# Optimization experiments

Hardware: AMD Instinct MI355X
Metric: run time of the kernel (lower is better)

The kernel has to match this reference:

```python
import jax, jax.numpy as jnp
import numpy as np

B, M, L, HID, H, LAYERS = 16, 128, 512, 256, 4, 2
DH = HID // H  # 64 = head dim, also kernel_param dim


def _ln(x, g, b, eps=1e-5):
    mu = jnp.mean(x, axis=-1, keepdims=True)
    var = jnp.mean((x - mu) ** 2, axis=-1, keepdims=True)
    return (x - mu) / jnp.sqrt(var + eps) * g + b


def setup_inputs() -> dict:
    key = jax.random.key(0)
    ks = jax.random.split(key, 24)
    s = 0.05
    return {
        "ct_t": jax.random.uniform(ks[0], (B, M), jnp.float32),
        "ts_t": jax.random.uniform(ks[1], (B, L), jnp.float32),
        "ct_emb": jax.random.normal(ks[2], (B, M, HID), jnp.float32),
        "ts_emb": jax.random.normal(ks[3], (B, L, HID), jnp.float32),
        "kernel_param": jax.random.normal(ks[4], (DH,), jnp.float32),
        "ct_W": jax.random.normal(ks[5], (HID, HID), jnp.float32) * s,
        "ct_b": jnp.zeros((HID,), jnp.float32),
        "fW0": jax.random.normal(ks[6], (HID, HID), jnp.float32) * s,
        "fb0": jnp.zeros((HID,), jnp.float32),
        "fW1": jax.random.normal(ks[7], (HID, HID), jnp.float32) * s,
        "fb1": jnp.zeros((HID,), jnp.float32),
        "fW2": jax.random.normal(ks[8], (HID, HID), jnp.float32) * s,
        "fb2": jnp.zeros((HID,), jnp.float32),
        "f_ln_g": jnp.ones((HID,), jnp.float32),
        "f_ln_b": jnp.zeros((HID,), jnp.float32),
        "Wqkv": jax.random.normal(ks[9], (LAYERS, 3 * HID, HID), jnp.float32) * s,
        "bqkv": jnp.zeros((LAYERS, 3 * HID), jnp.float32),
        "Wo": jax.random.normal(ks[10], (LAYERS, HID, HID), jnp.float32) * s,
        "bo": jnp.zeros((LAYERS, HID), jnp.float32),
        "W1": jax.random.normal(ks[11], (LAYERS, 2 * HID, HID), jnp.float32) * s,
        "b1": jnp.zeros((LAYERS, 2 * HID), jnp.float32),
        "W2": jax.random.normal(ks[12], (LAYERS, HID, 2 * HID), jnp.float32) * s,
        "b2": jnp.zeros((LAYERS, HID), jnp.float32),
        "ln1_g": jnp.ones((LAYERS, HID), jnp.float32),
        "ln1_b": jnp.zeros((LAYERS, HID), jnp.float32),
        "ln2_g": jnp.ones((LAYERS, HID), jnp.float32),
        "ln2_b": jnp.zeros((LAYERS, HID), jnp.float32),
        "pred_W": jax.random.normal(ks[13], (1, HID), jnp.float32) * s,
        "pred_b": jnp.zeros((1,), jnp.float32),
    }


def reference(ct_t, ts_t, ct_emb, ts_emb, kernel_param, ct_W, ct_b,
              fW0, fb0, fW1, fb1, fW2, fb2, f_ln_g, f_ln_b,
              Wqkv, bqkv, Wo, bo, W1, b1, W2, b2,
              ln1_g, ln1_b, ln2_g, ln2_b, pred_W, pred_b):
    # --- TN tokenizer: multi-scale RBF kernel temporal fusion ---
    alpha = jax.nn.softplus(kernel_param)                       # [DH]  log(1+exp(p))
    ct_e = (jnp.einsum('bmd,ed->bme', ct_emb, ct_W) + ct_b)     # [B,M,HID]
    ct_e = ct_e.reshape(B, M, H, DH)
    diff = ct_t[:, :, None] - ts_t[:, None, :]                  # [B,M,L]
    norm = (diff * diff)[..., None]                             # [B,M,L,1]
    outs = []
    for s in range(H):                                          # fixed small loop over scales
        z = (-float(s)) * alpha * norm                          # [B,M,L,DH]
        w = jax.nn.logsumexp(z, axis=3, keepdims=True)          # [B,M,L,1]
        sim = jnp.exp(z - w)                                    # normalized kernel sims
        outs.append(jnp.einsum('bmnd,bmd->bnd', sim, ct_e[:, :, s, :]))  # scatter over ts events
    temp = jnp.concatenate(outs, axis=-1)                       # [B,L,HID]
    # --- Fusion module ---
    aux = jax.nn.elu(temp @ fW0.T + fb0 + ts_emb @ fW1.T + fb1)
    x = _ln(aux @ fW2.T + fb2 + ts_emb, f_ln_g, f_ln_b)         # [B,L,HID]
    # --- Transformer encoder (post-LN, gelu, no dropout at eval) ---
    inv_sqrt = 1.0 / np.sqrt(DH).astype(np.float32)
    for l in range(LAYERS):
        qkv = x @ Wqkv[l].T + bqkv[l]                           # [B,L,3*HID]
        q, k, v = jnp.split(qkv, 3, axis=-1)
        def heads(t):
            return t.reshape(B, L, H, DH).transpose(0, 2, 1, 3)
        q, k, v = heads(q), heads(k), heads(v)
        att = jax.nn.softmax(jnp.einsum('bhqd,bhkd->bhqk', q, k) * inv_sqrt, axis=-1)
        o = jnp.einsum('bhqk,bhkd->bhqd', att, v).transpose(0, 2, 1, 3).reshape(B, L, HID)
        x = _ln(x + o @ Wo[l].T + bo[l], ln1_g[l], ln1_b[l])
        ff = jax.nn.gelu(x @ W1[l].T + b1[l], approximate=False) @ W2[l].T + b2[l]
        x = _ln(x + ff, ln2_g[l], ln2_b[l])
    return x @ pred_W.T + pred_b                                # [B,L,1]
```

## Files before the change

### kernel.cpp

```cpp
#include <hip/hip_runtime.h>
#include <hip/hip_bf16.h>
#include <cstddef>

#define Bsz 16
#define Msz 128
#define Lsz 512
#define HIDs 256

typedef __attribute__((ext_vector_type(4))) float f32x4;
typedef __attribute__((ext_vector_type(8))) __bf16 bf16x8;
typedef __attribute__((ext_vector_type(8))) unsigned short ushort8;

#define CHEB_K 12
#define PI_F 3.14159265358979323846f

static __device__ inline unsigned short f2bf(float f) {
    __hip_bfloat16 h = __float2bfloat16(f);
    return *(unsigned short*)&h;
}
static __device__ inline float bf2f(unsigned short u) {
    return __builtin_bit_cast(float, (unsigned)u << 16);
}
static __device__ inline void gload16(const ushort* g, ushort* l) {
    __builtin_amdgcn_global_load_lds(
        (const __attribute__((address_space(1))) void*)g,
        (__attribute__((address_space(3))) void*)l, 16, 0, 0);
}

__global__ __launch_bounds__(256) void cvt_all_kernel(
    const float* __restrict__ ts_emb, const float* __restrict__ ct_emb,
    const float* __restrict__ ct_W, const float* __restrict__ fW0,
    const float* __restrict__ fW1, const float* __restrict__ fW2,
    const float* __restrict__ Wqkv, const float* __restrict__ Wo,
    const float* __restrict__ W1, const float* __restrict__ W2,
    ushort* __restrict__ Xcat, ushort* __restrict__ Wcat,
    ushort* __restrict__ cebin, ushort* __restrict__ wct,
    ushort* __restrict__ wf2, ushort* __restrict__ wqkv,
    ushort* __restrict__ wo, ushort* __restrict__ w1, ushort* __restrict__ w2)
{
    const unsigned u = blockIdx.x * 256u + threadIdx.x;
    const float* src; ushort* dst; unsigned rel;
    if (u < 262144u) {
        rel = u; src = ts_emb;
        dst = Xcat + ((size_t)(rel >> 5) * 512 + 256 + (rel & 31) * 8);
    } else if (u < 327680u) { rel = u - 262144u; src = ct_emb; dst = cebin + (size_t)rel * 8; }
    else if (u < 335872u) { rel = u - 327680u; src = ct_W; dst = wct + (size_t)rel * 8; }
    else if (u < 344064u) { rel = u - 335872u; src = fW0;
        dst = Wcat + ((size_t)(rel >> 5) * 512 + (rel & 31) * 8); }
    else if (u < 352256u) { rel = u - 344064u; src = fW1;
        dst = Wcat + ((size_t)(rel >> 5) * 512 + 256 + (rel & 31) * 8); }
    else if (u < 360448u) { rel = u - 352256u; src = fW2; dst = wf2 + (size_t)rel * 8; }
    else if (u < 409600u) { rel = u - 360448u; src = Wqkv; dst = wqkv + (size_t)rel * 8; }
    else if (u < 425984u) { rel = u - 409600u; src = Wo;  dst = wo + (size_t)rel * 8; }
    else if (u < 458752u) { rel = u - 425984u; src = W1;  dst = w1 + (size_t)rel * 8; }
    else                  { rel = u - 458752u; src = W2;  dst = w2 + (size_t)rel * 8; }
    float4 a = ((const float4*)src)[(size_t)rel * 2];
    float4 b = ((const float4*)src)[(size_t)rel * 2 + 1];
    ushort8 o;
    o[0] = f2bf(a.x); o[1] = f2bf(a.y); o[2] = f2bf(a.z); o[3] = f2bf(a.w);
    o[4] = f2bf(b.x); o[5] = f2bf(b.y); o[6] = f2bf(b.z); o[7] = f2bf(b.w);
    *(ushort8*)dst = o;
}

__global__ __launch_bounds__(256) void gemm_mfma_kernel(
    const ushort* __restrict__ X, const ushort* __restrict__ W,
    const float* __restrict__ bias, const float* __restrict__ bias2,
    float* __restrict__ Yf, ushort* __restrict__ Yb,
    int NR, int K, int OUT, int act)
{
    __shared__ ushort As[64 * 64];
    __shared__ ushort Bs[128 * 64];

    const int nbx = OUT >> 7;
    const int bx = blockIdx.x % nbx;
    const int by = blockIdx.x / nbx;
    const int r0 = by << 6, o0 = bx << 7;
    const int tid = threadIdx.x;
    const int w = tid >> 6;
    const int lane = tid & 63;
    const int wr = w >> 1, wc = w & 1;
    const int lr = lane & 15, lg = lane >> 4;

    const int grow = lane >> 3;
    const int gchunk = (lane & 7) ^ grow;

    unsigned aoff[2][2], boff[4][2];
    #pragma unroll
    for (int f = 0; f < 2; f++) {
        unsigned cc = (unsigned)((lg + 4 * f) ^ (lr & 7)) * 16u;
        #pragma unroll
        for (int m = 0; m < 2; m++)
            aoff[m][f] = (unsigned)(wr * 32 + m * 16 + lr) * 128u + cc;
        #pragma unroll
        for (int n = 0; n < 4; n++)
            boff[n][f] = (unsigned)(wc * 64 + n * 16 + lr) * 128u + cc;
    }

    f32x4 acc[2][4];
    #pragma unroll
    for (int m = 0; m < 2; m++)
        #pragma unroll
        for (int n = 0; n < 4; n++) acc[m][n] = (f32x4){0.f, 0.f, 0.f, 0.f};

    const int nk = K >> 6;
    for (int ks = 0; ks < nk; ks++) {
        const int k0 = ks << 6;
        if (ks) __syncthreads();
        #pragma unroll
        for (int i = 0; i < 2; i++) {
            int row = w * 16 + i * 8 + grow;
            gload16(X + (size_t)(r0 + row) * K + k0 + gchunk * 8,
                    &As[(w * 16 + i * 8) * 64]);
        }
        #pragma unroll
        for (int i = 0; i < 4; i++) {
            int row = w * 32 + i * 8 + grow;
            gload16(W + (size_t)(o0 + row) * K + k0 + gchunk * 8,
                    &Bs[(w * 32 + i * 8) * 64]);
        }
        __syncthreads();

        #pragma unroll
        for (int f = 0; f < 2; f++) {
            bf16x8 av[2], bv[4];
            #pragma unroll
            for (int m = 0; m < 2; m++)
                av[m] = *(const bf16x8*)((const char*)As + aoff[m][f]);
            #pragma unroll
            for (int n = 0; n < 4; n++)
                bv[n] = *(const bf16x8*)((const char*)Bs + boff[n][f]);
            #pragma unroll
            for (int m = 0; m < 2; m++)
                #pragma unroll
                for (int n = 0; n < 4; n++)
                    acc[m][n] = __builtin_amdgcn_mfma_f32_16x16x32_bf16(
                        av[m], bv[n], acc[m][n], 0, 0, 0);
        }
    }

    const int ocol0 = o0 + wc * 64;
    float bn[4];
    #pragma unroll
    for (int n = 0; n < 4; n++) {
        int o = ocol0 + n * 16 + lr;
        bn[n] = bias[o] + (bias2 ? bias2[o] : 0.f);
    }

    #pragma unroll
    for (int m = 0; m < 2; m++) {
        #pragma unroll
        for (int p = 0; p < 4; p++) {
            int r = r0 + wr * 32 + m * 16 + 4 * lg + p;
            size_t rb = (size_t)r * OUT;
            #pragma unroll
            for (int n = 0; n < 4; n++) {
                int o = ocol0 + n * 16 + lr;
                float v = acc[m][n][p] + bn[n];
                if (act == 1)      v = (v > 0.f) ? v : (__expf(v) - 1.f);
                else if (act == 2) v = 0.5f * v * (1.f + erff(v * 0.70710678118654752f));
                if (Yf) Yf[rb + o] = v;
                if (Yb) Yb[rb + o] = f2bf(v);
            }
        }
    }
}

__global__ __launch_bounds__(256) void gemm_ln_kernel(
    const ushort* __restrict__ X, const ushort* __restrict__ W,
    const float* __restrict__ bias, const float* __restrict__ add,
    const float* __restrict__ lng, const float* __restrict__ lnb,
    float* __restrict__ Xf, ushort* __restrict__ Xb,
    const float* __restrict__ predW, const float* __restrict__ predb,
    float* __restrict__ pout, int K)
{
    __shared__ ushort As[32 * 64];
    __shared__ ushort Bs[256 * 64];
    __shared__ float redA[32][4];
    __shared__ float redB[32][4];

    const int r0 = blockIdx.x << 5;
    const int tid = threadIdx.x;
    const int w = tid >> 6;
    const int lane = tid & 63;
    const int lr = lane & 15, lg = lane >> 4;
    const int grow = lane >> 3;
    const int gchunk = (lane & 7) ^ grow;

    unsigned aoff[2][2], boff[4][2];
    #pragma unroll
    for (int f = 0; f < 2; f++) {
        unsigned cc = (unsigned)((lg + 4 * f) ^ (lr & 7)) * 16u;
        #pragma unroll
        for (int m = 0; m < 2; m++)
            aoff[m][f] = (unsigned)(m * 16 + lr) * 128u + cc;
        #pragma unroll
        for (int n = 0; n < 4; n++)
            boff[n][f] = (unsigned)(w * 64 + n * 16 + lr) * 128u + cc;
    }

    f32x4 acc[2][4];
    #pragma unroll
    for (int m = 0; m < 2; m++)
        #pragma unroll
        for (int n = 0; n < 4; n++) acc[m][n] = (f32x4){0.f, 0.f, 0.f, 0.f};

    const int nk = K >> 6;
    for (int ks = 0; ks < nk; ks++) {
        const int k0 = ks << 6;
        if (ks) __syncthreads();
        gload16(X + (size_t)(r0 + w * 8 + grow) * K + k0 + gchunk * 8,
                &As[(w * 8) * 64]);
        #pragma unroll
        for (int i = 0; i < 8; i++) {
            gload16(W + (size_t)(w * 64 + i * 8 + grow) * K + k0 + gchunk * 8,
                    &Bs[(w * 64 + i * 8) * 64]);
        }
        __syncthreads();

        #pragma unroll
        for (int f = 0; f < 2; f++) {
            bf16x8 av[2], bv[4];
            #pragma unroll
            for (int m = 0; m < 2; m++)
                av[m] = *(const bf16x8*)((const char*)As + aoff[m][f]);
            #pragma unroll
            for (int n = 0; n < 4; n++)
                bv[n] = *(const bf16x8*)((const char*)Bs + boff[n][f]);
            #pragma unroll
            for (int m = 0; m < 2; m++)
                #pragma unroll
                for (int n = 0; n < 4; n++)
                    acc[m][n] = __builtin_amdgcn_mfma_f32_16x16x32_bf16(
                        av[m], bv[n], acc[m][n], 0, 0, 0);
        }
    }

    const int col0 = w * 64;
    float bn[4], gv[4], bv2[4], pwv[4];
    #pragma unroll
    for (int n = 0; n < 4; n++) {
        int o = col0 + n * 16 + lr;
        bn[n] = bias[o];
        gv[n] = lng[o];
        bv2[n] = lnb[o];
        pwv[n] = predW ? predW[o] : 0.f;
    }
    #pragma unroll
    for (int m = 0; m < 2; m++)
        #pragma unroll
        for (int p = 0; p < 4; p++) {
            int r = r0 + m * 16 + 4 * lg + p;
            size_t rb = (size_t)r * 256;
            #pragma unroll
            for (int n = 0; n < 4; n++)
                acc[m][n][p] += bn[n] + add[rb + col0 + n * 16 + lr];
        }

    #pragma unroll
    for (int m = 0; m < 2; m++)
        #pragma unroll
        for (int p = 0; p < 4; p++) {
            float s = acc[m][0][p] + acc[m][1][p] + acc[m][2][p] + acc[m][3][p];
            #pragma unroll
            for (int o = 1; o <= 8; o <<= 1) s += __shfl_xor(s, o);
            if (lr == 0) redA[m * 16 + 4 * lg + p][w] = s;
        }
    __syncthreads();
    float mu[2][4];
    #pragma unroll
    for (int m = 0; m < 2; m++)
        #pragma unroll
        for (int p = 0; p < 4; p++) {
            int row = m * 16 + 4 * lg + p;
            mu[m][p] = (redA[row][0] + redA[row][1] + redA[row][2] + redA[row][3])
                       * (1.f / 256.f);
        }

    #pragma unroll
    for (int m = 0; m < 2; m++)
        #pragma unroll
        for (int p = 0; p < 4; p++) {
            float q = 0.f;
            #pragma unroll
            for (int n = 0; n < 4; n++) {
                float dl = acc[m][n][p] - mu[m][p];
                q = fmaf(dl, dl, q);
            }
            #pragma unroll
            for (int o = 1; o <= 8; o <<= 1) q += __shfl_xor(q, o);
            if (lr == 0) redB[m * 16 + 4 * lg + p][w] = q;
        }
    __syncthreads();

    #pragma unroll
    for (int m = 0; m < 2; m++)
        #pragma unroll
        for (int p = 0; p < 4; p++) {
            int row = m * 16 + 4 * lg + p;
            float var = (redB[row][0] + redB[row][1] + redB[row][2] + redB[row][3])
                        * (1.f / 256.f);
            float rsig = rsqrtf(var + 1e-5f);
            int r = r0 + row;
            size_t rb = (size_t)r * 256;
            float pd = 0.f;
            #pragma unroll
            for (int n = 0; n < 4; n++) {
                int o = col0 + n * 16 + lr;
                float xn = (acc[m][n][p] - mu[m][p]) * rsig * gv[n] + bv2[n];
                if (Xf) Xf[rb + o] = xn;
                if (Xb) Xb[rb + o] = f2bf(xn);
                pd = fmaf(xn, pwv[n], pd);
            }
            if (predW) {
                #pragma unroll
                for (int o = 1; o <= 8; o <<= 1) pd += __shfl_xor(pd, o);
                if (lr == 0) redA[row][w] = pd;
            }
        }
    if (predW) {
        __syncthreads();
        if (tid < 32)
            pout[r0 + tid] = redA[tid][0] + redA[tid][1] + redA[tid][2]
                           + redA[tid][3] + predb[0];
    }
}

__global__ __launch_bounds__(256) void cheb_kernel(
    const float* __restrict__ kp, float* __restrict__ clut, float* __restrict__ cD)
{
    __shared__ float costab[CHEB_K][32];
    __shared__ float xq[32];
    __shared__ float alph[64];
    const int t = threadIdx.x;
    if (t < 64) {
        float p = kp[t];
        alph[t] = fmaxf(p, 0.f) + log1pf(__expf(-fabsf(p)));
    }
    #pragma unroll
    for (int i = 0; i < 2; i++) {
        int idx = i * 256 + t;
        if (idx < CHEB_K * 32) {
            int k = idx >> 5, q = idx & 31;
            float th = (q + 0.5f) * (PI_F / 32.f);
            costab[k][q] = __cosf((float)k * th);
        }
    }
    if (t < 32) xq[t] = 0.5f * (1.f + __cosf((t + 0.5f) * (PI_F / 32.f)));
    __syncthreads();

    if (t >= 192) return;
    const int d = t & 63, s1 = t >> 6;
    const float u = (float)(s1 + 1) * alph[d];
    float f[32];
    #pragma unroll
    for (int q = 0; q < 32; q++) f[q] = __expf(-u * xq[q]);
    #pragma unroll
    for (int k = 0; k < CHEB_K; k++) {
        float sum = 0.f;
        #pragma unroll
        for (int q = 0; q < 32; q++) sum = fmaf(f[q], costab[k][q], sum);
        float c = sum * ((k == 0 ? 1.f : 2.f) / 32.f);
        clut[s1 * (CHEB_K * 64) + k * 64 + d] = c;
        float sr = c;
        #pragma unroll
        for (int o = 1; o <= 32; o <<= 1) sr += __shfl_xor(sr, o, 64);
        if (d == 0) cD[s1 * CHEB_K + k] = sr;
    }
}

__global__ __launch_bounds__(256) void denom3_kernel(
    const float* __restrict__ ct_t, const float* __restrict__ ts_t,
    const float* __restrict__ cD, ushort* __restrict__ invW)
{
    __shared__ float cd[3][CHEB_K];
    const int tid = threadIdx.x;
    if (tid < 3 * CHEB_K) cd[tid / CHEB_K][tid % CHEB_K] = cD[tid];
    __syncthreads();

    const unsigned G = blockIdx.x * 256u + tid;
    const int b = G >> 16;
    const int n = (G >> 7) & 511;
    const int m = G & 127;

    float x = ct_t[b * Msz + m] - ts_t[b * Lsz + n];
    x = x * x;
    const float xi = 2.f * x - 1.f;
    const float xi2 = 2.f * xi;

    float t0 = 1.f, t1 = xi;
    float a1 = cd[0][0] + cd[0][1] * xi;
    float a2 = cd[1][0] + cd[1][1] * xi;
    float a3 = cd[2][0] + cd[2][1] * xi;
    #pragma unroll
    for (int k = 2; k < CHEB_K; k++) {
        float tn = fmaf(xi2, t1, -t0);
        a1 = fmaf(cd[0][k], tn, a1);
        a2 = fmaf(cd[1][k], tn, a2);
        a3 = fmaf(cd[2][k], tn, a3);
        t0 = t1; t1 = tn;
    }
    const size_t base = ((size_t)b * 3 * Lsz + n) * Msz + m;
    invW[base]                         = f2bf(1.f / a1);
    invW[base + (size_t)Lsz * Msz]     = f2bf(1.f / a2);
    invW[base + (size_t)2 * Lsz * Msz] = f2bf(1.f / a3);
}

__global__ __launch_bounds__(256) void tok3_kernel(
    const float* __restrict__ ct_t, const float* __restrict__ ts_t,
    const ushort* __restrict__ ceb, const ushort* __restrict__ invW,
    const float* __restrict__ clut, ushort* __restrict__ Xcat)
{
    const int bid = blockIdx.x;
    const int nt = bid & 7;
    const int s1 = (bid >> 3) % 3;
    const int b  = bid / 24;
    const int tid = threadIdx.x;
    const int w = tid >> 6, lane = tid & 63, g = lane >> 4, r = lane & 15;

    __shared__ ushort ceT[64][136];
    __shared__ float  cl[CHEB_K][64];
    __shared__ float  cts[128];

    #pragma unroll
    for (int i = 0; i < 8; i++) {
        int idx = i * 256 + tid;
        int m = idx >> 4, d4 = (idx & 15) << 2;
        const ushort* gp = ceb + (((size_t)b * 128 + m) << 8) + (s1 + 1) * 64 + d4;
        ushort4 v = *(const ushort4*)gp;
        ceT[d4 + 0][m] = v.x; ceT[d4 + 1][m] = v.y;
        ceT[d4 + 2][m] = v.z; ceT[d4 + 3][m] = v.w;
    }
    #pragma unroll
    for (int i = 0; i < 3; i++) {
        int idx = i * 256 + tid;
        cl[idx >> 6][idx & 63] = clut[s1 * (CHEB_K * 64) + idx];
    }
    if (tid < 128) cts[tid] = ct_t[b * 128 + tid];
    __syncthreads();

    const int nrow = nt * 64 + w * 16 + r;
    const float tsn = ts_t[b * 512 + nrow];

    float xi2v[4][8], Ta[4][8], Tb[4][8];
    #pragma unroll
    for (int t4 = 0; t4 < 4; t4++) {
        int m0 = 8 * g + 32 * t4;
        ushort8 iv = *(const ushort8*)&invW[((((size_t)b * 3 + s1) * 512 + nrow) << 7) + m0];
        #pragma unroll
        for (int j = 0; j < 8; j++) {
            float dfx = cts[m0 + j] - tsn;
            float x = dfx * dfx;
            float xi = 2.f * x - 1.f;
            float w0 = bf2f(iv[j]);
            xi2v[t4][j] = 2.f * xi;
            Ta[t4][j] = w0;
            Tb[t4][j] = w0 * xi;
        }
    }

    bf16x8 cef[4][4];
    #pragma unroll
    for (int db = 0; db < 4; db++)
        #pragma unroll
        for (int t4 = 0; t4 < 4; t4++)
            cef[db][t4] = *(const bf16x8*)&ceT[db * 16 + r][8 * g + 32 * t4];

    f32x4 acc[4];
    #pragma unroll
    for (int db = 0; db < 4; db++) acc[db] = (f32x4){0.f, 0.f, 0.f, 0.f};

    #pragma unroll
    for (int k = 0; k < CHEB_K; k++) {
        if (k >= 2) {
            #pragma unroll
            for (int t4 = 0; t4 < 4; t4++)
                #pragma unroll
                for (int j = 0; j < 8; j++) {
                    if (k & 1) Tb[t4][j] = fmaf(xi2v[t4][j], Ta[t4][j], -Tb[t4][j]);
                    else       Ta[t4][j] = fmaf(xi2v[t4][j], Tb[t4][j], -Ta[t4][j]);
                }
        }
        bf16x8 af[4];
        #pragma unroll
        for (int t4 = 0; t4 < 4; t4++) {
            ushort8 u;
            #pragma unroll
            for (int j = 0; j < 8; j++)
                u[j] = f2bf((k & 1) ? Tb[t4][j] : Ta[t4][j]);
            af[t4] = __builtin_bit_cast(bf16x8, u);
        }
        #pragma unroll
        for (int db = 0; db < 4; db++) {
            f32x4 gk = (f32x4){0.f, 0.f, 0.f, 0.f};
            #pragma unroll
            for (int t4 = 0; t4 < 4; t4++)
                gk = __builtin_amdgcn_mfma_f32_16x16x32_bf16(af[t4], cef[db][t4], gk, 0, 0, 0);
            float ck = cl[k][db * 16 + r];
            #pragma unroll
            for (int p = 0; p < 4; p++) acc[db][p] = fmaf(ck, gk[p], acc[db][p]);
        }
    }

    #pragma unroll
    for (int db = 0; db < 4; db++)
        #pragma unroll
        for (int p = 0; p < 4; p++) {
            int n_out = nt * 64 + w * 16 + 4 * g + p;
            Xcat[((size_t)b * 512 + n_out) * 512 + (s1 + 1) * 64 + db * 16 + r] =
                f2bf(acc[db][p]);
        }
}

__global__ __launch_bounds__(256) void bcast0_kernel(
    const ushort* __restrict__ ceb, ushort* __restrict__ Xcat)
{
    const int b = blockIdx.x;
    const int t = threadIdx.x;
    const int d = t & 63, q = t >> 6;
    float s = 0.f;
    #pragma unroll 8
    for (int i = 0; i < 32; i++) {
        int m = q * 32 + i;
        s += bf2f(ceb[(((size_t)b * 128 + m) << 8) + d]);
    }
    __shared__ float red[4][64];
    __shared__ ushort row[64];
    red[q][d] = s;
    __syncthreads();
    if (t < 64)
        row[t] = f2bf((red[0][t] + red[1][t] + red[2][t] + red[3][t]) * (1.f / 64.f));
    __syncthreads();
    #pragma unroll
    for (int i = 0; i < 16; i++) {
        int idx = i * 256 + t;
        int n = idx >> 3, j = idx & 7;
        *(ushort8*)&Xcat[((size_t)b * 512 + n) * 512 + j * 8] =
            *(const ushort8*)&row[j * 8];
    }
}

__global__ __launch_bounds__(256) void attn_mfma_kernel(
    const ushort* __restrict__ qkv, ushort* __restrict__ Ob)
{
    const int bid = blockIdx.x;
    const int qt = bid & 7;
    const int h  = (bid >> 3) & 3;
    const int b  = bid >> 5;
    const int t  = threadIdx.x;
    const int w  = t >> 6;
    const int lane = t & 63;
    const int g = lane >> 4;
    const int r = lane & 15;

    __shared__ ushort Ks[64][72];
    __shared__ ushort Vt[64][72];
    __shared__ float  Ps[4][16][65];

    const ushort* base = qkv + (size_t)b * Lsz * 768;
    const int q0 = qt * 64 + w * 16;

    bf16x8 qf[2];
    {
        const ushort* qp = base + (size_t)(q0 + r) * 768 + h * 64 + 8 * g;
        qf[0] = __builtin_bit_cast(bf16x8, *(const ushort8*)qp);
        qf[1] = __builtin_bit_cast(bf16x8, *(const ushort8*)(qp + 32));
    }

    f32x4 Ofr[4];
    #pragma unroll
    for (int dblk = 0; dblk < 4; dblk++) Ofr[dblk] = (f32x4){0.f, 0.f, 0.f, 0.f};
    float m_run[4] = {-1e30f, -1e30f, -1e30f, -1e30f};
    float l_run[4] = {0.f, 0.f, 0.f, 0.f};

    const int srow = t >> 2;
    const int sseg = t & 3;

    for (int c = 0; c < 8; c++) {
        __syncthreads();
        {
            const ushort* kr = base + (size_t)(c * 64 + srow) * 768 + 256 + h * 64 + sseg * 16;
            ushort8 k0 = *(const ushort8*)kr;
            ushort8 k1 = *(const ushort8*)(kr + 8);
            *(ushort8*)&Ks[srow][sseg * 16]     = k0;
            *(ushort8*)&Ks[srow][sseg * 16 + 8] = k1;
            ushort8 v0 = *(const ushort8*)(kr + 256);
            ushort8 v1 = *(const ushort8*)(kr + 264);
            #pragma unroll
            for (int j = 0; j < 8; j++) {
                Vt[sseg * 16 + j][srow]     = v0[j];
                Vt[sseg * 16 + 8 + j][srow] = v1[j];
            }
        }
        __syncthreads();

        f32x4 sfr[4];
        #pragma unroll
        for (int s = 0; s < 4; s++) {
            f32x4 a2 = (f32x4){0.f, 0.f, 0.f, 0.f};
            #pragma unroll
            for (int f = 0; f < 2; f++) {
                bf16x8 kf = *(const bf16x8*)&Ks[s * 16 + r][8 * g + 32 * f];
                a2 = __builtin_amdgcn_mfma_f32_16x16x32_bf16(qf[f], kf, a2, 0, 0, 0);
            }
            #pragma unroll
            for (int p = 0; p < 4; p++) a2[p] *= 0.125f;
            sfr[s] = a2;
        }

        #pragma unroll
        for (int p = 0; p < 4; p++) {
            float rm = fmaxf(fmaxf(sfr[0][p], sfr[1][p]), fmaxf(sfr[2][p], sfr[3][p]));
            #pragma unroll
            for (int o = 1; o <= 8; o <<= 1) rm = fmaxf(rm, __shfl_xor(rm, o));
            float mnew = fmaxf(m_run[p], rm);
            float sc = __expf(m_run[p] - mnew);
            m_run[p] = mnew;
            float rs = 0.f;
            #pragma unroll
            for (int s = 0; s < 4; s++) {
                float pv = __expf(sfr[s][p] - mnew);
                Ps[w][4 * g + p][s * 16 + r] = pv;
                rs += pv;
            }
            #pragma unroll
            for (int o = 1; o <= 8; o <<= 1) rs += __shfl_xor(rs, o);
            l_run[p] = l_run[p] * sc + rs;
            #pragma unroll
            for (int dblk = 0; dblk < 4; dblk++) Ofr[dblk][p] *= sc;
        }

        __asm__ volatile("s_waitcnt lgkmcnt(0)" ::: "memory");

        #pragma unroll
        for (int f = 0; f < 2; f++) {
            const float* pp = &Ps[w][r][8 * g + 32 * f];
            ushort8 ua;
            #pragma unroll
            for (int j = 0; j < 8; j++) ua[j] = f2bf(pp[j]);
            bf16x8 pa = __builtin_bit_cast(bf16x8, ua);
            #pragma unroll
            for (int dblk = 0; dblk < 4; dblk++) {
                bf16x8 vb = *(const bf16x8*)&Vt[dblk * 16 + r][32 * f + 8 * g];
                Ofr[dblk] = __builtin_amdgcn_mfma_f32_16x16x32_bf16(
                    pa, vb, Ofr[dblk], 0, 0, 0);
            }
        }
    }

    #pragma unroll
    for (int dblk = 0; dblk < 4; dblk++) {
        #pragma unroll
        for (int p = 0; p < 4; p++) {
            int row = q0 + 4 * g + p;
            Ob[(size_t)(b * Lsz + row) * HIDs + h * 64 + dblk * 16 + r] =
                f2bf(Ofr[dblk][p] / l_run[p]);
        }
    }
}

extern "C" void kernel_launch(void* const* d_in, const int* in_sizes, int n_in,
                              void* d_out, int out_size, void* d_ws, size_t ws_size,
                              hipStream_t stream)
{
    (void)in_sizes; (void)n_in; (void)out_size; (void)ws_size;

    const float* ct_t   = (const float*)d_in[0];
    const float* ts_t   = (const float*)d_in[1];
    const float* ct_emb = (const float*)d_in[2];
    const float* ts_emb = (const float*)d_in[3];
    const float* kp     = (const float*)d_in[4];
    const float* ct_W   = (const float*)d_in[5];
    const float* ct_b   = (const float*)d_in[6];
    const float* fW0    = (const float*)d_in[7];
    const float* fb0    = (const float*)d_in[8];
    const float* fW1    = (const float*)d_in[9];
    const float* fb1    = (const float*)d_in[10];
    const float* fW2    = (const float*)d_in[11];
    const float* fb2    = (const float*)d_in[12];
    const float* f_ln_g = (const float*)d_in[13];
    const float* f_ln_b = (const float*)d_in[14];
    const float* Wqkv   = (const float*)d_in[15];
    const float* bqkv   = (const float*)d_in[16];
    const float* Wo     = (const float*)d_in[17];
    const float* bo     = (const float*)d_in[18];
    const float* W1     = (const float*)d_in[19];
    const float* b1     = (const float*)d_in[20];
    const float* W2     = (const float*)d_in[21];
    const float* b2     = (const float*)d_in[22];
    const float* ln1_g  = (const float*)d_in[23];
    const float* ln1_b  = (const float*)d_in[24];
    const float* ln2_g  = (const float*)d_in[25];
    const float* ln2_b  = (const float*)d_in[26];
    const float* pred_W = (const float*)d_in[27];
    const float* pred_b = (const float*)d_in[28];

    ushort* wsb = (ushort*)d_ws;
    ushort* invW  = wsb;
    ushort* auxbf = wsb;
    ushort* qkvbf = wsb;
    ushort* ff1bf = wsb;
    ushort* Xcat  = wsb + 12582912;
    ushort* Wcat  = wsb + 16777216;
    ushort* cebin = wsb + 16908288;
    ushort* cebout= wsb + 17432576;
    ushort* wct   = wsb + 17956864;
    ushort* wf2   = wsb + 18022400;
    ushort* wqkv  = wsb + 18087936;
    ushort* wo    = wsb + 18481152;
    ushort* w1    = wsb + 18612224;
    ushort* w2    = wsb + 18874368;
    ushort* xbf   = wsb + 19136512;
    ushort* obf   = wsb + 21233664;
    float*  wsf   = (float*)d_ws;
    float*  xbuf  = wsf + 11665408;
    float*  clut  = wsf + 13762560;
    float*  cDp   = wsf + 13764864;

    const int NRts = Bsz * Lsz;
    const int NRct = Bsz * Msz;
    auto grid = [](int nr, int out) { return dim3((unsigned)((nr >> 6) * (out >> 7))); };

    cvt_all_kernel<<<dim3(1920), 256, 0, stream>>>(
        ts_emb, ct_emb, ct_W, fW0, fW1, fW2, Wqkv, Wo, W1, W2,
        Xcat, Wcat, cebin, wct, wf2, wqkv, wo, w1, w2);

    gemm_mfma_kernel<<<grid(NRct, 256), 256, 0, stream>>>(
        cebin, wct, ct_b, nullptr, nullptr, cebout, NRct, 256, 256, 0);
    cheb_kernel<<<dim3(1), 256, 0, stream>>>(kp, clut, cDp);
    denom3_kernel<<<dim3(Bsz * Msz * Lsz / 256), 256, 0, stream>>>(ct_t, ts_t, cDp, invW);
    tok3_kernel<<<dim3(384), 256, 0, stream>>>(ct_t, ts_t, cebout, invW, clut, Xcat);
    bcast0_kernel<<<dim3(Bsz), 256, 0, stream>>>(cebout, Xcat);

    gemm_mfma_kernel<<<grid(NRts, 256), 256, 0, stream>>>(
        Xcat, Wcat, fb0, fb1, nullptr, auxbf, NRts, 512, 256, 1);
    gemm_ln_kernel<<<dim3(NRts / 32), 256, 0, stream>>>(
        auxbf, wf2, fb2, ts_emb, f_ln_g, f_ln_b, xbuf, xbf,
        nullptr, nullptr, nullptr, 256);

    for (int l = 0; l < 2; l++) {
        gemm_mfma_kernel<<<grid(NRts, 768), 256, 0, stream>>>(
            xbf, wqkv + (size_t)l * 196608, bqkv + l * 768, nullptr,
            nullptr, qkvbf, NRts, 256, 768, 0);
        attn_mfma_kernel<<<dim3(512), 256, 0, stream>>>(qkvbf, obf);
        gemm_ln_kernel<<<dim3(NRts / 32), 256, 0, stream>>>(
            obf, wo + (size_t)l * 65536, bo + l * 256, xbuf,
            ln1_g + l * 256, ln1_b + l * 256, xbuf, xbf,
            nullptr, nullptr, nullptr, 256);
        gemm_mfma_kernel<<<grid(NRts, 512), 256, 0, stream>>>(
            xbf, w1 + (size_t)l * 131072, b1 + l * 512, nullptr,
            nullptr, ff1bf, NRts, 256, 512, 2);
        if (l == 0) {
            gemm_ln_kernel<<<dim3(NRts / 32), 256, 0, stream>>>(
                ff1bf, w2 + (size_t)l * 131072, b2 + l * 256, xbuf,
                ln2_g + l * 256, ln2_b + l * 256, xbuf, xbf,
                nullptr, nullptr, nullptr, 512);
        } else {
            gemm_ln_kernel<<<dim3(NRts / 32), 256, 0, stream>>>(
                ff1bf, w2 + (size_t)l * 131072, b2 + l * 256, xbuf,
                ln2_g + l * 256, ln2_b + l * 256, nullptr, nullptr,
                pred_W, pred_b, (float*)d_out, 512);
        }
    }
}
```

Baseline: 219.7 us.

## Double-buffer LDS tiles in GEMM and attention kernels to overlap loads with MFMA

Measured after the change: 218.4 us. Within noise of the previous version (-0.6%).

```diff
diff --git a/kernel.cpp b/kernel.cpp
--- a/kernel.cpp
+++ b/kernel.cpp
@@ -68,8 +68,8 @@
     float* __restrict__ Yf, ushort* __restrict__ Yb,
     int NR, int K, int OUT, int act)
 {
-    __shared__ ushort As[64 * 64];
-    __shared__ ushort Bs[128 * 64];
+    __shared__ ushort As[2][64 * 64];
+    __shared__ ushort Bs[2][128 * 64];
 
     const int nbx = OUT >> 7;
     const int bx = blockIdx.x % nbx;
@@ -103,32 +103,39 @@
         for (int n = 0; n < 4; n++) acc[m][n] = (f32x4){0.f, 0.f, 0.f, 0.f};
 
     const int nk = K >> 6;
-    for (int ks = 0; ks < nk; ks++) {
+
+    auto stage = [&](int buf, int ks) {
         const int k0 = ks << 6;
-        if (ks) __syncthreads();
         #pragma unroll
         for (int i = 0; i < 2; i++) {
             int row = w * 16 + i * 8 + grow;
             gload16(X + (size_t)(r0 + row) * K + k0 + gchunk * 8,
-                    &As[(w * 16 + i * 8) * 64]);
+                    &As[buf][(w * 16 + i * 8) * 64]);
         }
         #pragma unroll
         for (int i = 0; i < 4; i++) {
             int row = w * 32 + i * 8 + grow;
             gload16(W + (size_t)(o0 + row) * K + k0 + gchunk * 8,
-                    &Bs[(w * 32 + i * 8) * 64]);
-        }
-        __syncthreads();
-
+                    &Bs[buf][(w * 32 + i * 8) * 64]);
+        }
+    };
+
+    stage(0, 0);
+    __syncthreads();
+    int cur = 0;
+    for (int ks = 0; ks < nk; ks++) {
+        if (ks + 1 < nk) stage(cur ^ 1, ks + 1);
+        const char* Ab = (const char*)As[cur];
+        const char* Bb = (const char*)Bs[cur];
         #pragma unroll
         for (int f = 0; f < 2; f++) {
             bf16x8 av[2], bv[4];
             #pragma unroll
             for (int m = 0; m < 2; m++)
-                av[m] = *(const bf16x8*)((const char*)As + aoff[m][f]);
+                av[m] = *(const bf16x8*)(Ab + aoff[m][f]);
             #pragma unroll
             for (int n = 0; n < 4; n++)
-                bv[n] = *(const bf16x8*)((const char*)Bs + boff[n][f]);
+                bv[n] = *(const bf16x8*)(Bb + boff[n][f]);
             #pragma unroll
             for (int m = 0; m < 2; m++)
                 #pragma unroll
@@ -136,6 +143,8 @@
                     acc[m][n] = __builtin_amdgcn_mfma_f32_16x16x32_bf16(
                         av[m], bv[n], acc[m][n], 0, 0, 0);
         }
+        __syncthreads();
+        cur ^= 1;
     }
 
     const int ocol0 = o0 + wc * 64;
@@ -173,8 +182,8 @@
     const float* __restrict__ predW, const float* __restrict__ predb,
     float* __restrict__ pout, int K)
 {
-    __shared__ ushort As[32 * 64];
-    __shared__ ushort Bs[256 * 64];
+    __shared__ ushort As[2][32 * 64];
+    __shared__ ushort Bs[2][256 * 64];
     __shared__ float redA[32][4];
     __shared__ float redB[32][4];
 
@@ -205,27 +214,34 @@
         for (int n = 0; n < 4; n++) acc[m][n] = (f32x4){0.f, 0.f, 0.f, 0.f};
 
     const int nk = K >> 6;
-    for (int ks = 0; ks < nk; ks++) {
+
+    auto stage = [&](int buf, int ks) {
         const int k0 = ks << 6;
-        if (ks) __syncthreads();
         gload16(X + (size_t)(r0 + w * 8 + grow) * K + k0 + gchunk * 8,
-                &As[(w * 8) * 64]);
+                &As[buf][(w * 8) * 64]);
         #pragma unroll
         for (int i = 0; i < 8; i++) {
             gload16(W + (size_t)(w * 64 + i * 8 + grow) * K + k0 + gchunk * 8,
-                    &Bs[(w * 64 + i * 8) * 64]);
-        }
-        __syncthreads();
-
+                    &Bs[buf][(w * 64 + i * 8) * 64]);
+        }
+    };
+
+    stage(0, 0);
+    __syncthreads();
+    int cur = 0;
+    for (int ks = 0; ks < nk; ks++) {
+        if (ks + 1 < nk) stage(cur ^ 1, ks + 1);
+        const char* Ab = (const char*)As[cur];
+        const char* Bb = (const char*)Bs[cur];
         #pragma unroll
         for (int f = 0; f < 2; f++) {
             bf16x8 av[2], bv[4];
             #pragma unroll
             for (int m = 0; m < 2; m++)
-                av[m] = *(const bf16x8*)((const char*)As + aoff[m][f]);
+                av[m] = *(const bf16x8*)(Ab + aoff[m][f]);
             #pragma unroll
             for (int n = 0; n < 4; n++)
-                bv[n] = *(const bf16x8*)((const char*)Bs + boff[n][f]);
+                bv[n] = *(const bf16x8*)(Bb + boff[n][f]);
             #pragma unroll
             for (int m = 0; m < 2; m++)
                 #pragma unroll
@@ -233,6 +249,8 @@
                     acc[m][n] = __builtin_amdgcn_mfma_f32_16x16x32_bf16(
                         av[m], bv[n], acc[m][n], 0, 0, 0);
         }
+        __syncthreads();
+        cur ^= 1;
     }
 
     const int col0 = w * 64;
@@ -552,8 +570,8 @@
     const int g = lane >> 4;
     const int r = lane & 15;
 
-    __shared__ ushort Ks[64][72];
-    __shared__ ushort Vt[64][72];
+    __shared__ ushort Ks[2][64][72];
+    __shared__ ushort Vt[2][64][72];
     __shared__ float  Ps[4][16][65];
 
     const ushort* base = qkv + (size_t)b * Lsz * 768;
@@ -575,23 +593,31 @@
     const int srow = t >> 2;
     const int sseg = t & 3;
 
+    ushort8 pk0, pk1, pv0, pv1;
+    auto gload_chunk = [&](int c) {
+        const ushort* kr = base + (size_t)(c * 64 + srow) * 768 + 256 + h * 64 + sseg * 16;
+        pk0 = *(const ushort8*)kr;
+        pk1 = *(const ushort8*)(kr + 8);
+        pv0 = *(const ushort8*)(kr + 256);
+        pv1 = *(const ushort8*)(kr + 264);
+    };
+    auto write_chunk = [&](int buf) {
+        *(ushort8*)&Ks[buf][srow][sseg * 16]     = pk0;
+        *(ushort8*)&Ks[buf][srow][sseg * 16 + 8] = pk1;
+        #pragma unroll
+        for (int j = 0; j < 8; j++) {
+            Vt[buf][sseg * 16 + j][srow]     = pv0[j];
+            Vt[buf][sseg * 16 + 8 + j][srow] = pv1[j];
+        }
+    };
+
+    gload_chunk(0);
+    write_chunk(0);
+    __syncthreads();
+    int cur = 0;
+
     for (int c = 0; c < 8; c++) {
-        __syncthreads();
-        {
-            const ushort* kr = base + (size_t)(c * 64 + srow) * 768 + 256 + h * 64 + sseg * 16;
-            ushort8 k0 = *(const ushort8*)kr;
-            ushort8 k1 = *(const ushort8*)(kr + 8);
-            *(ushort8*)&Ks[srow][sseg * 16]     = k0;
-            *(ushort8*)&Ks[srow][sseg * 16 + 8] = k1;
-            ushort8 v0 = *(const ushort8*)(kr + 256);
-            ushort8 v1 = *(const ushort8*)(kr + 264);
-            #pragma unroll
-            for (int j = 0; j < 8; j++) {
-                Vt[sseg * 16 + j][srow]     = v0[j];
-                Vt[sseg * 16 + 8 + j][srow] = v1[j];
-            }
-        }
-        __syncthreads();
+        if (c < 7) gload_chunk(c + 1);
 
         f32x4 sfr[4];
         #pragma unroll
@@ -599,7 +625,7 @@
             f32x4 a2 = (f32x4){0.f, 0.f, 0.f, 0.f};
             #pragma unroll
             for (int f = 0; f < 2; f++) {
-                bf16x8 kf = *(const bf16x8*)&Ks[s * 16 + r][8 * g + 32 * f];
+                bf16x8 kf = *(const bf16x8*)&Ks[cur][s * 16 + r][8 * g + 32 * f];
                 a2 = __builtin_amdgcn_mfma_f32_16x16x32_bf16(qf[f], kf, a2, 0, 0, 0);
             }
             #pragma unroll
@@ -640,11 +666,15 @@
             bf16x8 pa = __builtin_bit_cast(bf16x8, ua);
             #pragma unroll
             for (int dblk = 0; dblk < 4; dblk++) {
-                bf16x8 vb = *(const bf16x8*)&Vt[dblk * 16 + r][32 * f + 8 * g];
+                bf16x8 vb = *(const bf16x8*)&Vt[cur][dblk * 16 + r][32 * f + 8 * g];
                 Ofr[dblk] = __builtin_amdgcn_mfma_f32_16x16x32_bf16(
                     pa, vb, Ofr[dblk], 0, 0, 0);
             }
         }
+
+        if (c < 7) write_chunk(cur ^ 1);
+        __syncthreads();
+        cur ^= 1;
     }
 
     #pragma unroll
```
